# Kernel tuning notes

Measured on AMD Instinct MI355X. Metric: run time of the kernel, lower is better.

## Reference

```python
import jax, jax.numpy as jnp
import numpy as np

N_LEVELS = 12
N_FEATURES = 2
LOG2_T = 19
T = 2 ** LOG2_T
BASE_RES = 16
GROWTH = 1.38
RESOLUTIONS = [int(np.floor(BASE_RES * GROWTH ** l)) for l in range(N_LEVELS)]
N_PTS = 1048576

# primes as uint32; XOR/mod-2^19 only depend on low bits, so uint32 wraparound
# multiplication reproduces torch's int64 hash exactly.
P1 = np.uint32(2654435761)
P2 = np.uint32(805459861)

_OFFSETS = jnp.array([[0,0,0],[1,0,0],[0,1,0],[1,1,0],[0,0,1],[1,0,1],[0,1,1],[1,1,1]], dtype=jnp.uint32)  # (8,3)


def setup_inputs() -> dict:
    key = jax.random.key(0)
    k1, k2 = jax.random.split(key)
    x = jax.random.uniform(k1, (N_PTS, 3), dtype=jnp.float32)  # coords in [0,1]
    tables = jax.random.uniform(k2, (N_LEVELS, T, N_FEATURES), dtype=jnp.float32,
                                minval=-1e-4, maxval=1e-4)
    return {"x": x, "tables": tables}


def _encode(x, tables):
    res_arr = jnp.array(RESOLUTIONS, dtype=jnp.float32)  # (L,)

    def level_fn(table, res):
        x_scaled = x * res                      # (N,3)
        x_floor = jnp.floor(x_scaled)
        w = x_scaled - x_floor                  # (N,3) trilinear fractions
        xi = x_floor.astype(jnp.uint32)
        corners = xi[:, None, :] + _OFFSETS[None, :, :]          # (N,8,3)
        h = corners[..., 0] ^ (corners[..., 1] * P1) ^ (corners[..., 2] * P2)
        idx = (h & jnp.uint32(T - 1)).astype(jnp.int32)          # mod 2^19
        feats = table[idx]                                        # (N,8,F) gather
        # weight per corner: prod over dims of (w if offset==1 else 1-w)
        wc = jnp.where(_OFFSETS[None, :, :] == 1, w[:, None, :], 1.0 - w[:, None, :])
        weights = wc.prod(axis=-1)                                # (N,8)
        return (weights[..., None] * feats).sum(axis=1)           # (N,F)

    feats = jax.vmap(level_fn)(tables, res_arr)                   # (L,N,F)
    return feats.transpose(1, 0, 2).reshape(x.shape[0], -1)       # (N, L*F)


def reference(x, tables):
    return _encode(x, tables)
```

## Files before the change

### kernel.cpp

```cpp
#include <hip/hip_runtime.h>


constexpr int NPTS     = 1 << 20;
constexpr int NLEVELS  = 12;
constexpr unsigned T     = 1u << 19;
constexpr unsigned TMASK = T - 1u;
constexpr unsigned P1 = 2654435761u;
constexpr unsigned P2 = 805459861u;

typedef float vfloat2 __attribute__((ext_vector_type(2)));
typedef float vfloat4 __attribute__((ext_vector_type(4)));

__constant__ float c_res[NLEVELS] = {16.f, 22.f, 30.f, 42.f, 58.f, 80.f,
                                     110.f, 152.f, 210.f, 290.f, 400.f, 553.f};

__device__ __forceinline__ float2 encode_one_level(
    float px, float py, float pz, float r, const float2* __restrict__ tab)
{
    const float xs = px * r, ys = py * r, zs = pz * r;
    const float xf = floorf(xs), yf = floorf(ys), zf = floorf(zs);
    const float wx = xs - xf, wy = ys - yf, wz = zs - zf;
    const unsigned xi = (unsigned)xf, yi = (unsigned)yf, zi = (unsigned)zf;

    unsigned idx[8];
#pragma unroll
    for (int c = 0; c < 8; ++c) {
        const unsigned ox = c & 1u, oy = (c >> 1) & 1u, oz = (c >> 2) & 1u;
        const unsigned h = (xi + ox) ^ ((yi + oy) * P1) ^ ((zi + oz) * P2);
        idx[c] = h & TMASK;
    }
    float2 f[8];
#pragma unroll
    for (int c = 0; c < 8; ++c) f[c] = tab[idx[c]];

    float f0 = 0.f, f1 = 0.f;
#pragma unroll
    for (int c = 0; c < 8; ++c) {
        const unsigned ox = c & 1u, oy = (c >> 1) & 1u, oz = (c >> 2) & 1u;
        const float w = (ox ? wx : 1.f - wx) *
                        (oy ? wy : 1.f - wy) *
                        (oz ? wz : 1.f - wz);
        f0 += w * f[c].x;
        f1 += w * f[c].y;
    }
    return make_float2(f0, f1);
}

__global__ __launch_bounds__(256, 8)
void hashgrid_level_kernel(const float* __restrict__ x,
                           const float* __restrict__ tables,
                           float2* __restrict__ ws)
{
    const int n = blockIdx.x * 256 + threadIdx.x;
    const int l = blockIdx.y;

    const float px = x[3 * n + 0];
    const float py = x[3 * n + 1];
    const float pz = x[3 * n + 2];

    const float2* __restrict__ tab =
        reinterpret_cast<const float2*>(tables) + (size_t)l * T;

    const float2 f = encode_one_level(px, py, pz, c_res[l], tab);
    vfloat2 v = {f.x, f.y};
    __builtin_nontemporal_store(
        v, reinterpret_cast<vfloat2*>(&ws[(size_t)l * NPTS + n]));
}

__global__ __launch_bounds__(256, 8)
void hashgrid_transpose_kernel(const float2* __restrict__ ws,
                               float* __restrict__ out)
{
    __shared__ float lds[256 * 25];
    const int t = threadIdx.x;
    const int base = blockIdx.x * 256;

#pragma unroll
    for (int l = 0; l < NLEVELS; ++l) {
        const vfloat2 f = __builtin_nontemporal_load(
            reinterpret_cast<const vfloat2*>(&ws[(size_t)l * NPTS + base + t]));
        lds[t * 25 + 2 * l + 0] = f.x;
        lds[t * 25 + 2 * l + 1] = f.y;
    }
    __syncthreads();

    float* __restrict__ ob = out + (size_t)base * 24;
#pragma unroll
    for (int i = 0; i < 6; ++i) {
        const int j  = i * 256 + t;
        const int f0 = 4 * j;
        const int p  = f0 / 24;
        const int c  = f0 % 24;
        vfloat4 v = {lds[p * 25 + c + 0], lds[p * 25 + c + 1],
                     lds[p * 25 + c + 2], lds[p * 25 + c + 3]};
        __builtin_nontemporal_store(v, reinterpret_cast<vfloat4*>(ob + f0));
    }
}

__global__ __launch_bounds__(256, 4)
void hashgrid_fused_kernel(const float* __restrict__ x,
                           const float* __restrict__ tables,
                           float* __restrict__ out)
{
    const int n = blockIdx.x * 256 + threadIdx.x;
    const float px = x[3 * n + 0];
    const float py = x[3 * n + 1];
    const float pz = x[3 * n + 2];

    float o[2 * NLEVELS];
#pragma unroll
    for (int l = 0; l < NLEVELS; ++l) {
        const float2* __restrict__ tab =
            reinterpret_cast<const float2*>(tables) + (size_t)l * T;
        const float2 f = encode_one_level(px, py, pz, c_res[l], tab);
        o[2 * l + 0] = f.x;
        o[2 * l + 1] = f.y;
    }
    float4* __restrict__ op = reinterpret_cast<float4*>(out + (size_t)n * 24);
#pragma unroll
    for (int i = 0; i < 6; ++i)
        op[i] = make_float4(o[4*i+0], o[4*i+1], o[4*i+2], o[4*i+3]);
}

extern "C" void kernel_launch(void* const* d_in, const int* in_sizes, int n_in,
                              void* d_out, int out_size, void* d_ws, size_t ws_size,
                              hipStream_t stream)
{
    const float* x      = reinterpret_cast<const float*>(d_in[0]);
    const float* tables = reinterpret_cast<const float*>(d_in[1]);
    float* out          = reinterpret_cast<float*>(d_out);

    const size_t ws_needed = (size_t)NLEVELS * NPTS * sizeof(float2);
    if (ws_size >= ws_needed) {
        float2* ws = reinterpret_cast<float2*>(d_ws);
        dim3 grid(NPTS / 256, NLEVELS);
        hashgrid_level_kernel<<<grid, 256, 0, stream>>>(x, tables, ws);
        hashgrid_transpose_kernel<<<NPTS / 256, 256, 0, stream>>>(ws, out);
    } else {
        hashgrid_fused_kernel<<<NPTS / 256, 256, 0, stream>>>(x, tables, out);
    }
}
```

Baseline: 410.0 us.

## Process four points per thread in level kernel and two in transpose

The per-level encode kernel now handles four points per thread. It loads their coordinates with three 16-byte vector loads and writes the results with two 16-byte nontemporal stores, which puts 32 independent gathers in flight per thread. The transpose kernel now handles 512 points per block with 16-byte workspace loads and a doubled LDS buffer. The aim is fewer, wider memory instructions and more memory-level parallelism per thread. The cost is higher register use (launch bounds lowered to 4), lower occupancy, and fewer blocks, which can reduce latency hiding for the random table gathers.

```diff
diff --git a/kernel.cpp b/kernel.cpp
--- a/kernel.cpp
+++ b/kernel.cpp
@@ -46,47 +46,60 @@
     return make_float2(f0, f1);
 }
 
-__global__ __launch_bounds__(256, 8)
+__global__ __launch_bounds__(256, 4)
 void hashgrid_level_kernel(const float* __restrict__ x,
                            const float* __restrict__ tables,
                            float2* __restrict__ ws)
 {
-    const int n = blockIdx.x * 256 + threadIdx.x;
-    const int l = blockIdx.y;
+    const int t  = blockIdx.x * 256 + threadIdx.x;
+    const int l  = blockIdx.y;
+    const int n0 = t * 4;
 
-    const float px = x[3 * n + 0];
-    const float py = x[3 * n + 1];
-    const float pz = x[3 * n + 2];
-
+    const float r = c_res[l];
     const float2* __restrict__ tab =
         reinterpret_cast<const float2*>(tables) + (size_t)l * T;
 
-    const float2 f = encode_one_level(px, py, pz, c_res[l], tab);
-    vfloat2 v = {f.x, f.y};
-    __builtin_nontemporal_store(
-        v, reinterpret_cast<vfloat2*>(&ws[(size_t)l * NPTS + n]));
+    const vfloat4* __restrict__ xp =
+        reinterpret_cast<const vfloat4*>(x + (size_t)3 * n0);
+    const vfloat4 xa = xp[0], xb = xp[1], xc = xp[2];
+    const float px[4] = {xa.x, xa.w, xb.z, xc.y};
+    const float py[4] = {xa.y, xb.x, xb.w, xc.z};
+    const float pz[4] = {xa.z, xb.y, xc.x, xc.w};
+
+    float2 f[4];
+#pragma unroll
+    for (int p = 0; p < 4; ++p)
+        f[p] = encode_one_level(px[p], py[p], pz[p], r, tab);
+
+    float2* wp = &ws[(size_t)l * NPTS + n0];
+    vfloat4 v0 = {f[0].x, f[0].y, f[1].x, f[1].y};
+    vfloat4 v1 = {f[2].x, f[2].y, f[3].x, f[3].y};
+    __builtin_nontemporal_store(v0, reinterpret_cast<vfloat4*>(wp));
+    __builtin_nontemporal_store(v1, reinterpret_cast<vfloat4*>(wp) + 1);
 }
 
-__global__ __launch_bounds__(256, 8)
+__global__ __launch_bounds__(256)
 void hashgrid_transpose_kernel(const float2* __restrict__ ws,
                                float* __restrict__ out)
 {
-    __shared__ float lds[256 * 25];
+    __shared__ float lds[512 * 25];
     const int t = threadIdx.x;
-    const int base = blockIdx.x * 256;
+    const int base = blockIdx.x * 512;
 
 #pragma unroll
     for (int l = 0; l < NLEVELS; ++l) {
-        const vfloat2 f = __builtin_nontemporal_load(
-            reinterpret_cast<const vfloat2*>(&ws[(size_t)l * NPTS + base + t]));
-        lds[t * 25 + 2 * l + 0] = f.x;
-        lds[t * 25 + 2 * l + 1] = f.y;
+        const vfloat4 f = __builtin_nontemporal_load(
+            reinterpret_cast<const vfloat4*>(&ws[(size_t)l * NPTS + base + 2 * t]));
+        lds[(2 * t + 0) * 25 + 2 * l + 0] = f.x;
+        lds[(2 * t + 0) * 25 + 2 * l + 1] = f.y;
+        lds[(2 * t + 1) * 25 + 2 * l + 0] = f.z;
+        lds[(2 * t + 1) * 25 + 2 * l + 1] = f.w;
     }
     __syncthreads();
 
     float* __restrict__ ob = out + (size_t)base * 24;
 #pragma unroll
-    for (int i = 0; i < 6; ++i) {
+    for (int i = 0; i < 12; ++i) {
         const int j  = i * 256 + t;
         const int f0 = 4 * j;
         const int p  = f0 / 24;
@@ -133,9 +146,9 @@
     const size_t ws_needed = (size_t)NLEVELS * NPTS * sizeof(float2);
     if (ws_size >= ws_needed) {
         float2* ws = reinterpret_cast<float2*>(d_ws);
-        dim3 grid(NPTS / 256, NLEVELS);
+        dim3 grid(NPTS / 1024, NLEVELS);
         hashgrid_level_kernel<<<grid, 256, 0, stream>>>(x, tables, ws);
-        hashgrid_transpose_kernel<<<NPTS / 256, 256, 0, stream>>>(ws, out);
+        hashgrid_transpose_kernel<<<NPTS / 512, 256, 0, stream>>>(ws, out);
     } else {
         hashgrid_fused_kernel<<<NPTS / 256, 256, 0, stream>>>(x, tables, out);
     }
```

Measured after the change: 461.0 us. 1.12x slower.
